# Performance work log

Hardware: AMD Instinct MI355X
Metric: run time of the kernel (lower is better)

## Reference

```python
import jax, jax.numpy as jnp
import numpy as np

B_SZ, T, H, N, L = 4, 512, 256, 64, 4
EPS = 1e-5

def _hippo(n):
    i = np.arange(n)[:, None]; j = np.arange(n)[None, :]
    A = np.where(i >= j, ((-1.0) ** (i - j)) * np.sqrt((2 * i + 1.0) * (2 * j + 1.0)), 0.0)
    # scale to be contractive so the 512-step dense recurrence stays finite
    A = A / (1.1 * np.linalg.norm(A, 2))
    return A.astype(np.float32)

def _xavier(key, shape):
    fan_in, fan_out = shape[1], shape[0]
    a = float(np.sqrt(6.0 / (fan_in + fan_out)))
    return jax.random.uniform(key, shape, jnp.float32, -a, a)

def setup_inputs() -> dict:
    key = jax.random.key(0)
    ks = jax.random.split(key, 8)
    x = jax.random.normal(ks[0], (B_SZ, T, H), jnp.float32)
    A = jnp.broadcast_to(jnp.asarray(_hippo(N)), (L, N, N))
    Bm = jnp.stack([_xavier(jax.random.fold_in(ks[1], l), (N, H)) for l in range(L)])
    Cm = jnp.stack([_xavier(jax.random.fold_in(ks[2], l), (H, N)) for l in range(L)])
    Dm = jnp.stack([_xavier(jax.random.fold_in(ks[3], l), (H, H)) for l in range(L)])
    Win = _xavier(ks[4], (H, H)); bin_ = jnp.zeros((H,), jnp.float32)
    Wout = _xavier(ks[5], (H, H)); bout = jnp.zeros((H,), jnp.float32)
    return {"x": x, "Win": Win, "bin_": bin_, "Wout": Wout, "bout": bout,
            "A": A, "Bm": Bm, "Cm": Cm, "Dm": Dm}

def _ln(x):
    m = jnp.mean(x, -1, keepdims=True)
    v = jnp.mean((x - m) ** 2, -1, keepdims=True)
    return (x - m) / jnp.sqrt(v + EPS)

def _ssm_layer(h, A, B, C, D):
    # h: (B,T,H); dense state (B,N,H)
    Cbar = C.mean(0)            # mean over output rows (matches C_state.mean(dim=2))
    BT = B.T                    # (H,N)
    DT = D.T                    # (H,H)
    def step(state, u):        # state (B,N,H), u (B,H)
        y = jnp.einsum('bnh,n->bh', state, Cbar) + u @ DT   # output uses pre-update state
        new_state = jnp.einsum('nm,bmh->bnh', A, state) + (u @ BT)[:, :, None]
        return new_state, y
    state0 = jnp.zeros((h.shape[0], A.shape[0], h.shape[2]), h.dtype)
    _, ys = jax.lax.scan(step, state0, jnp.swapaxes(h, 0, 1))  # scan over T
    y = jnp.swapaxes(ys, 0, 1)
    y = jax.nn.gelu(y, approximate=False) + h   # GELU -> (dropout=0) -> residual
    return _ln(y)

def reference(x, Win, bin_, Wout, bout, A, Bm, Cm, Dm):
    h = x @ Win.T + bin_
    for l in range(L):
        h = _ssm_layer(h, A[l], Bm[l], Cm[l], Dm[l])
    h = _ln(h)
    return h @ Wout.T + bout
```

## Files before the change

kernel.cpp:

```cpp
#include <hip/hip_runtime.h>

#define TSEQ 512
#define HDIM 256
#define NDIM 64
#define LC   48
#define YSTR 260

typedef __attribute__((ext_vector_type(4))) float  f32x4;
typedef __attribute__((ext_vector_type(8))) short  s16x8;
typedef __attribute__((ext_vector_type(4))) unsigned short u16x4;
typedef unsigned long long u64;
typedef unsigned short us;

#define MFMA16 __builtin_amdgcn_mfma_f32_16x16x32_bf16

__device__ __forceinline__ float wave_red(float v) {
#pragma unroll
    for (int m = 1; m < 64; m <<= 1) v += __shfl_xor(v, m, 64);
    return v;
}
__device__ __forceinline__ float lane_bcast(float v, int l) {
    return __int_as_float(__builtin_amdgcn_readlane(__float_as_int(v), l));
}
__device__ __forceinline__ us f2bf(float f) {
    unsigned u = __float_as_uint(f);
    u += 0x7fffu + ((u >> 16) & 1u);
    return (us)(u >> 16);
}
__device__ __forceinline__ float bf2f(us h) {
    return __uint_as_float(((unsigned)h) << 16);
}
__device__ __forceinline__ int swz(int row, int chunk) {
    return row * 512 + (((chunk) ^ (row & 7)) << 4);
}

__global__ void __launch_bounds__(256) k_prep(
    const float* __restrict__ Win, const float* __restrict__ Wout,
    const float* __restrict__ Bm, const float* __restrict__ Dm,
    const float* __restrict__ Cm, const float* __restrict__ A,
    us* __restrict__ Win_bf, us* __restrict__ Wout_bf,
    us* __restrict__ Bm_bf, us* __restrict__ Dm_bf,
    float* __restrict__ cbar_g, float* __restrict__ wA8)
{
    __shared__ __align__(16) float Pa[4096];
    __shared__ __align__(16) float Pb[4096];
    const int gid = blockIdx.x, tid = threadIdx.x;

    if (gid < 128) {
        for (int q = gid * 256 + tid; q < 114688; q += 32768) {
            const float* s; us* d; int off;
            if (q < 16384)      { s = Win;  d = Win_bf;  off = q; }
            else if (q < 32768) { s = Wout; d = Wout_bf; off = q - 16384; }
            else if (q < 49152) { s = Bm;   d = Bm_bf;   off = q - 32768; }
            else                { s = Dm;   d = Dm_bf;   off = q - 49152; }
            f32x4 v = ((const f32x4*)s)[off];
            u16x4 p; p[0] = f2bf(v[0]); p[1] = f2bf(v[1]); p[2] = f2bf(v[2]); p[3] = f2bf(v[3]);
            ((u16x4*)d)[off] = p;
        }
        return;
    }
    if (gid == 128) {
        const int l = tid >> 6, n = tid & 63;
        const float* cp = Cm + (size_t)l * HDIM * NDIM + n;
        float s0 = 0.f, s1 = 0.f, s2 = 0.f, s3 = 0.f;
        for (int h = 0; h < HDIM; h += 4) {
            s0 += cp[(h + 0) * NDIM]; s1 += cp[(h + 1) * NDIM];
            s2 += cp[(h + 2) * NDIM]; s3 += cp[(h + 3) * NDIM];
        }
        cbar_g[tid] = ((s0 + s1) + (s2 + s3)) * (1.0f / HDIM);
        return;
    }
    for (int q = tid; q < 1024; q += 256) ((f32x4*)Pa)[q] = ((const f32x4*)A)[q];
    __syncthreads();
    const int r0 = (tid >> 3) * 2, c0 = (tid & 7) * 8;
    const f32x4 z4 = {0.f, 0.f, 0.f, 0.f};
#pragma unroll 1
    for (int it = 0; it < 3; ++it) {
        const float* S = (it & 1) ? Pb : Pa;
        float*       D = (it & 1) ? Pa : Pb;
        f32x4 s00 = z4, s01 = z4, s10 = z4, s11 = z4;
        for (int k = 0; k < 64; ++k) {
            float a0 = S[r0 * 64 + k], a1 = S[(r0 + 1) * 64 + k];
            f32x4 b0 = *(const f32x4*)(S + k * 64 + c0);
            f32x4 b1 = *(const f32x4*)(S + k * 64 + c0 + 4);
            s00 += a0 * b0; s01 += a0 * b1; s10 += a1 * b0; s11 += a1 * b1;
        }
        *(f32x4*)(D + r0 * 64 + c0) = s00;       *(f32x4*)(D + r0 * 64 + c0 + 4) = s01;
        *(f32x4*)(D + (r0 + 1) * 64 + c0) = s10; *(f32x4*)(D + (r0 + 1) * 64 + c0 + 4) = s11;
        __syncthreads();
    }
    for (int q = tid; q < 1024; q += 256) ((f32x4*)wA8)[q] = ((const f32x4*)Pb)[q];
}

__global__ void __launch_bounds__(512, 2) k_front(
    const float* __restrict__ x, const float* __restrict__ bin,
    const us* __restrict__ Win_bf, const us* __restrict__ Bm_bf,
    const float* __restrict__ A, const float* __restrict__ wA8,
    const float* __restrict__ cbar_g,
    us* __restrict__ hA, float* __restrict__ binpA, float* __restrict__ wbuf)
{
    __shared__ __align__(16) float sm[13312];
    us* xl = (us*)sm;

    const int gid = blockIdx.x, tid = threadIdx.x;
    const int lane = tid & 63, wv = tid >> 6;
    const int m = lane & 15, cgq = lane >> 4;
    const f32x4 z4 = {0.f, 0.f, 0.f, 0.f};

    if (gid == 128) {
        float* As  = sm;
        float* A8s = sm + 4096;
        float* uls = sm + 8192;
        for (int q = tid; q < 1024; q += 512) {
            ((f32x4*)As)[q]  = ((const f32x4*)A)[q];
            ((f32x4*)A8s)[q] = ((const f32x4*)wA8)[q];
        }
        __syncthreads();
        if (wv < 4) {
            const int l = wv;
            float u = cbar_g[l * 64 + lane];
            uls[(l * 8 + 0) * 64 + lane] = u;
#pragma unroll 1
            for (int s = 1; s < 8; ++s) {
                float p0 = 0.f, p1 = 0.f, p2 = 0.f, p3 = 0.f;
#pragma unroll
                for (int k = 0; k < 64; k += 4) {
                    p0 += As[(k + 0) * 64 + lane] * lane_bcast(u, k + 0);
                    p1 += As[(k + 1) * 64 + lane] * lane_bcast(u, k + 1);
                    p2 += As[(k + 2) * 64 + lane] * lane_bcast(u, k + 2);
                    p3 += As[(k + 3) * 64 + lane] * lane_bcast(u, k + 3);
                }
                u = (p0 + p1) + (p2 + p3);
                uls[(l * 8 + s) * 64 + lane] = u;
            }
        }
        __syncthreads();
        {
            const int p = wv;
            float u0 = uls[(0 * 8 + p) * 64 + lane];
            float u1 = uls[(1 * 8 + p) * 64 + lane];
            float u2 = uls[(2 * 8 + p) * 64 + lane];
            float u3 = uls[(3 * 8 + p) * 64 + lane];
#pragma unroll 1
            for (int k6 = 0; k6 < 6; ++k6) {
                const int j = p + 8 * k6;
                wbuf[(0 * LC + j) * 64 + lane] = u0;
                wbuf[(1 * LC + j) * 64 + lane] = u1;
                wbuf[(2 * LC + j) * 64 + lane] = u2;
                wbuf[(3 * LC + j) * 64 + lane] = u3;
                if (k6 < 5) {
                    float n0 = 0.f, n1 = 0.f, n2 = 0.f, n3 = 0.f;
#pragma unroll
                    for (int k = 0; k < 64; ++k) {
                        float a = A8s[k * 64 + lane];
                        n0 += a * lane_bcast(u0, k); n1 += a * lane_bcast(u1, k);
                        n2 += a * lane_bcast(u2, k); n3 += a * lane_bcast(u3, k);
                    }
                    u0 = n0; u1 = n1; u2 = n2; u3 = n3;
                }
            }
        }
        return;
    }

    const int b = gid >> 5, tb = gid & 31, t0 = tb * 16;
    const size_t grow = (size_t)(b * TSEQ + t0);

    {
        const f32x4* gs = (const f32x4*)(x + grow * HDIM);
#pragma unroll
        for (int k = 0; k < 2; ++k) {
            int q = tid + k * 512;
            int row = q >> 6, c4 = q & 63;
            f32x4 v = gs[q];
            u16x4 pk; pk[0] = f2bf(v[0]); pk[1] = f2bf(v[1]); pk[2] = f2bf(v[2]); pk[3] = f2bf(v[3]);
            *(u16x4*)((char*)xl + swz(row, c4 >> 1) + (c4 & 1) * 8) = pk;
        }
    }
    __syncthreads();

    {
        f32x4 accA = z4, accB = z4;
        const us* W0 = Win_bf + (size_t)(wv * 32 + m) * HDIM;
        const us* W1 = Win_bf + (size_t)(wv * 32 + 16 + m) * HDIM;
#pragma unroll
        for (int ks = 0; ks < 8; ++ks) {
            s16x8 av = *(const s16x8*)((const char*)xl + swz(m, ks * 4 + cgq));
            s16x8 b0 = *(const s16x8*)(W0 + ks * 32 + cgq * 8);
            s16x8 b1 = *(const s16x8*)(W1 + ks * 32 + cgq * 8);
            accA = MFMA16(av, b0, accA, 0, 0, 0);
            accB = MFMA16(av, b1, accB, 0, 0, 0);
        }
        __syncthreads();
        const int h0c = wv * 32 + m, h1c = wv * 32 + 16 + m;
        float bi0 = bin[h0c], bi1 = bin[h1c];
#pragma unroll
        for (int reg = 0; reg < 4; ++reg) {
            int trow = cgq * 4 + reg;
            *(us*)((char*)xl + swz(trow, h0c >> 3) + (h0c & 7) * 2) = f2bf(accA[reg] + bi0);
            *(us*)((char*)xl + swz(trow, h1c >> 3) + (h1c & 7) * 2) = f2bf(accB[reg] + bi1);
        }
    }
    __syncthreads();

    {
        us* gd = hA + grow * HDIM;
#pragma unroll
        for (int k = 0; k < 2; ++k) {
            int q = tid + k * 512;
            int row = q >> 6, c8 = q & 63;
            *(u16x4*)(gd + (size_t)row * HDIM + c8 * 4) =
                *(const u16x4*)((const char*)xl + swz(row, c8 >> 1) + (c8 & 1) * 8);
        }
    }
    if (wv < 4) {
        f32x4 accb = z4;
        const us* B0 = Bm_bf + (size_t)(wv * 16 + m) * HDIM;
#pragma unroll
        for (int ks = 0; ks < 8; ++ks) {
            s16x8 av = *(const s16x8*)((const char*)xl + swz(m, ks * 4 + cgq));
            s16x8 bv = *(const s16x8*)(B0 + ks * 32 + cgq * 8);
            accb = MFMA16(av, bv, accb, 0, 0, 0);
        }
#pragma unroll
        for (int reg = 0; reg < 4; ++reg)
            binpA[(grow + cgq * 4 + reg) * NDIM + wv * 16 + m] = accb[reg];
    }
}

template <bool LAST>
__global__ void __launch_bounds__(512, 2) k_layer(
    const us* __restrict__ hin, const float* __restrict__ binp_in,
    const float* __restrict__ wbuf_l, const us* __restrict__ Dl_bf,
    const us* __restrict__ Bn_bf, const us* __restrict__ Wout_bf,
    const float* __restrict__ bout,
    us* __restrict__ hout, float* __restrict__ binp_out, float* __restrict__ out)
{
    __shared__ __align__(16) us    xl[16 * HDIM];
    __shared__ __align__(16) float yl[16 * YSTR];
    __shared__ __align__(16) float bwin[64 * NDIM];
    __shared__ __align__(16) float wlds[LC * NDIM];
    __shared__ float cfin[16];

    const int gid = blockIdx.x, tid = threadIdx.x;
    const int lane = tid & 63, wv = tid >> 6;
    const int m = lane & 15, cgq = lane >> 4;
    const f32x4 z4 = {0.f, 0.f, 0.f, 0.f};
    const int b = gid >> 5, tb = gid & 31, t0 = tb * 16;
    const size_t grow = (size_t)(b * TSEQ + t0);

    {
        const us* gs = hin + grow * HDIM;
#pragma unroll
        for (int k = 0; k < 2; ++k) {
            int q = tid + k * 512;
            int row = q >> 6, c8 = q & 63;
            *(u16x4*)((char*)xl + swz(row, c8 >> 1) + (c8 & 1) * 8) =
                *(const u16x4*)(gs + (size_t)row * HDIM + c8 * 4);
        }
    }
    for (int q = tid; q < LC * NDIM / 4; q += 512)
        ((f32x4*)wlds)[q] = ((const f32x4*)wbuf_l)[q];
    {
        const u64* bi8 = (const u64*)(binp_in + (size_t)b * TSEQ * NDIM);
#pragma unroll
        for (int k = 0; k < 4; ++k) {
            int q = tid + k * 512;
            int r = q >> 5, cc = q & 31;
            int t = t0 - LC + r;
            ((u64*)bwin)[q] = (t >= 0) ? bi8[(size_t)t * 32 + cc] : 0ull;
        }
    }
    __syncthreads();

    f32x4 accA = z4, accB = z4;
    {
        const us* D0 = Dl_bf + (size_t)(wv * 32 + m) * HDIM;
        const us* D1 = Dl_bf + (size_t)(wv * 32 + 16 + m) * HDIM;
#pragma unroll
        for (int ks = 0; ks < 8; ++ks) {
            s16x8 av = *(const s16x8*)((const char*)xl + swz(m, ks * 4 + cgq));
            s16x8 b0 = *(const s16x8*)(D0 + ks * 32 + cgq * 8);
            s16x8 b1 = *(const s16x8*)(D1 + ks * 32 + cgq * 8);
            accA = MFMA16(av, b0, accA, 0, 0, 0);
            accB = MFMA16(av, b1, accB, 0, 0, 0);
        }
    }

    {
        const int r0 = wv * 2;
        float c0 = 0.f, c1 = 0.f;
        float v0 = bwin[(LC - 1 + r0) * NDIM + lane];
        float v1 = bwin[(LC + r0) * NDIM + lane];
#pragma unroll
        for (int j = 0; j < LC; ++j) {
            float wj = wlds[j * NDIM + lane];
            c0 += wj * v0; c1 += wj * v1;
            v1 = v0;
            int nr = LC - 2 + r0 - j; nr = nr < 0 ? 0 : nr;
            v0 = bwin[nr * NDIM + lane];
        }
        c0 = wave_red(c0); c1 = wave_red(c1);
        if (lane == 0) { cfin[r0] = c0; cfin[r0 + 1] = c1; }
    }
    __syncthreads();

#pragma unroll
    for (int nt = 0; nt < 2; ++nt) {
        int hcol = wv * 32 + nt * 16 + m;
#pragma unroll
        for (int reg = 0; reg < 4; ++reg) {
            int trow = cgq * 4 + reg;
            float val = (nt ? accB[reg] : accA[reg]) + cfin[trow];
            float g = 0.5f * val * (1.0f + erff(val * 0.70710678118654752f));
            float r = bf2f(*(const us*)((const char*)xl + swz(trow, hcol >> 3) + (hcol & 7) * 2));
            yl[trow * YSTR + hcol] = g + r;
        }
    }
    __syncthreads();

#pragma unroll
    for (int q = 0; q < 2; ++q) {
        int r = wv * 2 + q;
        f32x4 yv = *(const f32x4*)(yl + r * YSTR + lane * 4);
        float s = (yv[0] + yv[1]) + (yv[2] + yv[3]);
        float sq = yv[0] * yv[0] + yv[1] * yv[1] + yv[2] * yv[2] + yv[3] * yv[3];
        s = wave_red(s); sq = wave_red(sq);
        float mn = s * (1.0f / HDIM);
        float var = sq * (1.0f / HDIM) - mn * mn;
        float rs = rsqrtf(var + 1e-5f);
        if (LAST) { float vz = var * rs * rs; rs = rs * rsqrtf(vz + 1e-5f); }
        u16x4 zp;
        zp[0] = f2bf((yv[0] - mn) * rs); zp[1] = f2bf((yv[1] - mn) * rs);
        zp[2] = f2bf((yv[2] - mn) * rs); zp[3] = f2bf((yv[3] - mn) * rs);
        *(u16x4*)((char*)xl + swz(r, lane >> 1) + (lane & 1) * 8) = zp;
        if constexpr (!LAST)
            *(u16x4*)(hout + (grow + r) * HDIM + lane * 4) = zp;
    }
    __syncthreads();

    if constexpr (!LAST) {
        if (wv < 4) {
            f32x4 accb = z4;
            const us* B0 = Bn_bf + (size_t)(wv * 16 + m) * HDIM;
#pragma unroll
            for (int ks = 0; ks < 8; ++ks) {
                s16x8 av = *(const s16x8*)((const char*)xl + swz(m, ks * 4 + cgq));
                s16x8 bv = *(const s16x8*)(B0 + ks * 32 + cgq * 8);
                accb = MFMA16(av, bv, accb, 0, 0, 0);
            }
#pragma unroll
            for (int reg = 0; reg < 4; ++reg)
                binp_out[(grow + cgq * 4 + reg) * NDIM + wv * 16 + m] = accb[reg];
        }
    } else {
        f32x4 a2A = z4, a2B = z4;
        const us* W0 = Wout_bf + (size_t)(wv * 32 + m) * HDIM;
        const us* W1 = Wout_bf + (size_t)(wv * 32 + 16 + m) * HDIM;
#pragma unroll
        for (int ks = 0; ks < 8; ++ks) {
            s16x8 av = *(const s16x8*)((const char*)xl + swz(m, ks * 4 + cgq));
            s16x8 b0 = *(const s16x8*)(W0 + ks * 32 + cgq * 8);
            s16x8 b1 = *(const s16x8*)(W1 + ks * 32 + cgq * 8);
            a2A = MFMA16(av, b0, a2A, 0, 0, 0);
            a2B = MFMA16(av, b1, a2B, 0, 0, 0);
        }
#pragma unroll
        for (int nt = 0; nt < 2; ++nt) {
            int hcol = wv * 32 + nt * 16 + m;
            float bo = bout[hcol];
#pragma unroll
            for (int reg = 0; reg < 4; ++reg) {
                int trow = cgq * 4 + reg;
                out[(grow + trow) * HDIM + hcol] = (nt ? a2B[reg] : a2A[reg]) + bo;
            }
        }
    }
}

extern "C" void kernel_launch(void* const* d_in, const int* in_sizes, int n_in,
                              void* d_out, int out_size, void* d_ws, size_t ws_size,
                              hipStream_t stream) {
    (void)in_sizes; (void)n_in; (void)out_size; (void)ws_size;
    const float* x    = (const float*)d_in[0];
    const float* Win  = (const float*)d_in[1];
    const float* bin  = (const float*)d_in[2];
    const float* Wout = (const float*)d_in[3];
    const float* bout = (const float*)d_in[4];
    const float* A    = (const float*)d_in[5];
    const float* Bm   = (const float*)d_in[6];
    const float* Cm   = (const float*)d_in[7];
    const float* Dm   = (const float*)d_in[8];

    float* ws     = (float*)d_ws;
    float* wbuf   = ws;
    float* cbar_g = ws + 16384;
    float* wA8    = ws + 17408;
    float* biA    = ws + 21504;
    float* biB    = ws + 152576;
    us* Win_bf  = (us*)(ws + 283648);
    us* Wout_bf = Win_bf + 65536;
    us* Bm_bf   = Wout_bf + 65536;
    us* Dm_bf   = Bm_bf + 65536;
    us* hA      = Dm_bf + 262144;
    us* hB      = hA + 524288;
    float* out  = (float*)d_out;

    k_prep<<<130, 256, 0, stream>>>(Win, Wout, Bm, Dm, Cm, A,
                                    Win_bf, Wout_bf, Bm_bf, Dm_bf, cbar_g, wA8);
    k_front<<<129, 512, 0, stream>>>(x, bin, Win_bf, Bm_bf, A, wA8, cbar_g,
                                     hA, biA, wbuf);
    k_layer<false><<<128, 512, 0, stream>>>(hA, biA, wbuf + 0 * LC * NDIM,
        Dm_bf + (size_t)0 * 65536, Bm_bf + (size_t)1 * 16384, nullptr, nullptr,
        hB, biB, nullptr);
    k_layer<false><<<128, 512, 0, stream>>>(hB, biB, wbuf + 1 * LC * NDIM,
        Dm_bf + (size_t)1 * 65536, Bm_bf + (size_t)2 * 16384, nullptr, nullptr,
        hA, biA, nullptr);
    k_layer<false><<<128, 512, 0, stream>>>(hA, biA, wbuf + 2 * LC * NDIM,
        Dm_bf + (size_t)2 * 65536, Bm_bf + (size_t)3 * 16384, nullptr, nullptr,
        hB, biB, nullptr);
    k_layer<true><<<128, 512, 0, stream>>>(hB, biB, wbuf + 3 * LC * NDIM,
        Dm_bf + (size_t)3 * 65536, nullptr, Wout_bf, bout,
        nullptr, nullptr, out);
}
```

Measured before the change: 73.98 us.

## Fuse front and four layer kernels into one persistent kernel with flag sync

Merges the front projection and the four per-layer launches into a single kernel of 129 blocks. Each block keeps its 16-row activation tile in LDS across layers and waits only on agent-scope flags from the three preceding time blocks and from the kernel-weight block, instead of a full grid barrier at each launch boundary. This drops the bf16 h round-trips through global memory and four launch gaps. In exchange it relies on all 129 blocks being co-resident so the spin-waits cannot deadlock, and on relaxed atomics for cross-block visibility, which costs extra polling latency.

After: 71.94 us. 1.03x faster.

```diff
diff --git a/kernel.cpp b/kernel.cpp
--- a/kernel.cpp
+++ b/kernel.cpp
@@ -5,6 +5,7 @@
 #define NDIM 64
 #define LC   48
 #define YSTR 260
+#define NWB  128
 
 typedef __attribute__((ext_vector_type(4))) float  f32x4;
 typedef __attribute__((ext_vector_type(8))) short  s16x8;
@@ -32,6 +33,20 @@
 }
 __device__ __forceinline__ int swz(int row, int chunk) {
     return row * 512 + (((chunk) ^ (row & 7)) << 4);
+}
+
+__device__ __forceinline__ void st_mall(float* p, float v) {
+    __hip_atomic_store(p, v, __ATOMIC_RELAXED, __HIP_MEMORY_SCOPE_AGENT);
+}
+__device__ __forceinline__ u64 ld_mall8(const u64* p) {
+    return __hip_atomic_load(p, __ATOMIC_RELAXED, __HIP_MEMORY_SCOPE_AGENT);
+}
+__device__ __forceinline__ void flag_set(unsigned* f) {
+    __hip_atomic_store(f, 1u, __ATOMIC_RELAXED, __HIP_MEMORY_SCOPE_AGENT);
+}
+__device__ __forceinline__ void flag_wait(const unsigned* f) {
+    while (__hip_atomic_load(f, __ATOMIC_RELAXED, __HIP_MEMORY_SCOPE_AGENT) == 0u)
+        __builtin_amdgcn_s_sleep(1);
 }
 
 __global__ void __launch_bounds__(256) k_prep(
@@ -40,7 +55,8 @@
     const float* __restrict__ Cm, const float* __restrict__ A,
     us* __restrict__ Win_bf, us* __restrict__ Wout_bf,
     us* __restrict__ Bm_bf, us* __restrict__ Dm_bf,
-    float* __restrict__ cbar_g, float* __restrict__ wA8)
+    float* __restrict__ cbar_g, float* __restrict__ wA8,
+    unsigned* __restrict__ flags)
 {
     __shared__ __align__(16) float Pa[4096];
     __shared__ __align__(16) float Pb[4096];
@@ -60,6 +76,8 @@
         return;
     }
     if (gid == 128) {
+        for (int i = tid; i < 4 + 4 * NWB; i += 256)
+            __hip_atomic_store(&flags[i], 0u, __ATOMIC_RELAXED, __HIP_MEMORY_SCOPE_AGENT);
         const int l = tid >> 6, n = tid & 63;
         const float* cp = Cm + (size_t)l * HDIM * NDIM + n;
         float s0 = 0.f, s1 = 0.f, s2 = 0.f, s3 = 0.f;
@@ -92,25 +110,31 @@
     for (int q = tid; q < 1024; q += 256) ((f32x4*)wA8)[q] = ((const f32x4*)Pb)[q];
 }
 
-__global__ void __launch_bounds__(512, 2) k_front(
+__global__ void __launch_bounds__(512, 2) k_fused(
     const float* __restrict__ x, const float* __restrict__ bin,
-    const us* __restrict__ Win_bf, const us* __restrict__ Bm_bf,
-    const float* __restrict__ A, const float* __restrict__ wA8,
-    const float* __restrict__ cbar_g,
-    us* __restrict__ hA, float* __restrict__ binpA, float* __restrict__ wbuf)
+    const float* __restrict__ bout, const float* __restrict__ A,
+    const float* __restrict__ wA8, const float* __restrict__ cbar_g,
+    const us* __restrict__ Win_bf, const us* __restrict__ Wout_bf,
+    const us* __restrict__ Bm_bf, const us* __restrict__ Dm_bf,
+    float* __restrict__ wbuf, float* __restrict__ BiA, float* __restrict__ BiB,
+    unsigned* __restrict__ flags, float* __restrict__ out)
 {
-    __shared__ __align__(16) float sm[13312];
-    us* xl = (us*)sm;
+    __shared__ __align__(16) char smem[53568];
+    us*    xl   = (us*)smem;
+    float* yl   = (float*)(smem + 8192);
+    float* bwin = (float*)(smem + 24832);
+    float* wlds = (float*)(smem + 41216);
+    float* cfin = (float*)(smem + 53504);
 
     const int gid = blockIdx.x, tid = threadIdx.x;
     const int lane = tid & 63, wv = tid >> 6;
     const int m = lane & 15, cgq = lane >> 4;
     const f32x4 z4 = {0.f, 0.f, 0.f, 0.f};
 
-    if (gid == 128) {
-        float* As  = sm;
-        float* A8s = sm + 4096;
-        float* uls = sm + 8192;
+    if (gid == NWB) {
+        float* As  = (float*)smem;
+        float* A8s = (float*)(smem + 16384);
+        float* uls = (float*)(smem + 32768);
         for (int q = tid; q < 1024; q += 512) {
             ((f32x4*)As)[q]  = ((const f32x4*)A)[q];
             ((f32x4*)A8s)[q] = ((const f32x4*)wA8)[q];
@@ -144,10 +168,10 @@
 #pragma unroll 1
             for (int k6 = 0; k6 < 6; ++k6) {
                 const int j = p + 8 * k6;
-                wbuf[(0 * LC + j) * 64 + lane] = u0;
-                wbuf[(1 * LC + j) * 64 + lane] = u1;
-                wbuf[(2 * LC + j) * 64 + lane] = u2;
-                wbuf[(3 * LC + j) * 64 + lane] = u3;
+                st_mall(&wbuf[(0 * LC + j) * 64 + lane], u0);
+                st_mall(&wbuf[(1 * LC + j) * 64 + lane], u1);
+                st_mall(&wbuf[(2 * LC + j) * 64 + lane], u2);
+                st_mall(&wbuf[(3 * LC + j) * 64 + lane], u3);
                 if (k6 < 5) {
                     float n0 = 0.f, n1 = 0.f, n2 = 0.f, n3 = 0.f;
 #pragma unroll
@@ -160,6 +184,8 @@
                 }
             }
         }
+        __syncthreads();
+        if (tid < 4) flag_set(&flags[tid]);
         return;
     }
 
@@ -203,16 +229,6 @@
     }
     __syncthreads();
 
-    {
-        us* gd = hA + grow * HDIM;
-#pragma unroll
-        for (int k = 0; k < 2; ++k) {
-            int q = tid + k * 512;
-            int row = q >> 6, c8 = q & 63;
-            *(u16x4*)(gd + (size_t)row * HDIM + c8 * 4) =
-                *(const u16x4*)((const char*)xl + swz(row, c8 >> 1) + (c8 & 1) * 8);
-        }
-    }
     if (wv < 4) {
         f32x4 accb = z4;
         const us* B0 = Bm_bf + (size_t)(wv * 16 + m) * HDIM;
@@ -224,155 +240,143 @@
         }
 #pragma unroll
         for (int reg = 0; reg < 4; ++reg)
-            binpA[(grow + cgq * 4 + reg) * NDIM + wv * 16 + m] = accb[reg];
-    }
-}
-
-template <bool LAST>
-__global__ void __launch_bounds__(512, 2) k_layer(
-    const us* __restrict__ hin, const float* __restrict__ binp_in,
-    const float* __restrict__ wbuf_l, const us* __restrict__ Dl_bf,
-    const us* __restrict__ Bn_bf, const us* __restrict__ Wout_bf,
-    const float* __restrict__ bout,
-    us* __restrict__ hout, float* __restrict__ binp_out, float* __restrict__ out)
-{
-    __shared__ __align__(16) us    xl[16 * HDIM];
-    __shared__ __align__(16) float yl[16 * YSTR];
-    __shared__ __align__(16) float bwin[64 * NDIM];
-    __shared__ __align__(16) float wlds[LC * NDIM];
-    __shared__ float cfin[16];
-
-    const int gid = blockIdx.x, tid = threadIdx.x;
-    const int lane = tid & 63, wv = tid >> 6;
-    const int m = lane & 15, cgq = lane >> 4;
-    const f32x4 z4 = {0.f, 0.f, 0.f, 0.f};
-    const int b = gid >> 5, tb = gid & 31, t0 = tb * 16;
-    const size_t grow = (size_t)(b * TSEQ + t0);
-
-    {
-        const us* gs = hin + grow * HDIM;
-#pragma unroll
-        for (int k = 0; k < 2; ++k) {
-            int q = tid + k * 512;
-            int row = q >> 6, c8 = q & 63;
-            *(u16x4*)((char*)xl + swz(row, c8 >> 1) + (c8 & 1) * 8) =
-                *(const u16x4*)(gs + (size_t)row * HDIM + c8 * 4);
-        }
-    }
-    for (int q = tid; q < LC * NDIM / 4; q += 512)
-        ((f32x4*)wlds)[q] = ((const f32x4*)wbuf_l)[q];
-    {
-        const u64* bi8 = (const u64*)(binp_in + (size_t)b * TSEQ * NDIM);
-#pragma unroll
-        for (int k = 0; k < 4; ++k) {
-            int q = tid + k * 512;
-            int r = q >> 5, cc = q & 31;
-            int t = t0 - LC + r;
-            ((u64*)bwin)[q] = (t >= 0) ? bi8[(size_t)t * 32 + cc] : 0ull;
-        }
+            st_mall(&BiA[(grow + cgq * 4 + reg) * NDIM + wv * 16 + m], accb[reg]);
     }
     __syncthreads();
-
-    f32x4 accA = z4, accB = z4;
-    {
-        const us* D0 = Dl_bf + (size_t)(wv * 32 + m) * HDIM;
-        const us* D1 = Dl_bf + (size_t)(wv * 32 + 16 + m) * HDIM;
-#pragma unroll
-        for (int ks = 0; ks < 8; ++ks) {
-            s16x8 av = *(const s16x8*)((const char*)xl + swz(m, ks * 4 + cgq));
-            s16x8 b0 = *(const s16x8*)(D0 + ks * 32 + cgq * 8);
-            s16x8 b1 = *(const s16x8*)(D1 + ks * 32 + cgq * 8);
-            accA = MFMA16(av, b0, accA, 0, 0, 0);
-            accB = MFMA16(av, b1, accB, 0, 0, 0);
-        }
-    }
-
-    {
-        const int r0 = wv * 2;
-        float c0 = 0.f, c1 = 0.f;
-        float v0 = bwin[(LC - 1 + r0) * NDIM + lane];
-        float v1 = bwin[(LC + r0) * NDIM + lane];
-#pragma unroll
-        for (int j = 0; j < LC; ++j) {
-            float wj = wlds[j * NDIM + lane];
-            c0 += wj * v0; c1 += wj * v1;
-            v1 = v0;
-            int nr = LC - 2 + r0 - j; nr = nr < 0 ? 0 : nr;
-            v0 = bwin[nr * NDIM + lane];
-        }
-        c0 = wave_red(c0); c1 = wave_red(c1);
-        if (lane == 0) { cfin[r0] = c0; cfin[r0 + 1] = c1; }
-    }
-    __syncthreads();
-
-#pragma unroll
-    for (int nt = 0; nt < 2; ++nt) {
-        int hcol = wv * 32 + nt * 16 + m;
-#pragma unroll
-        for (int reg = 0; reg < 4; ++reg) {
-            int trow = cgq * 4 + reg;
-            float val = (nt ? accB[reg] : accA[reg]) + cfin[trow];
-            float g = 0.5f * val * (1.0f + erff(val * 0.70710678118654752f));
-            float r = bf2f(*(const us*)((const char*)xl + swz(trow, hcol >> 3) + (hcol & 7) * 2));
-            yl[trow * YSTR + hcol] = g + r;
-        }
-    }
-    __syncthreads();
-
-#pragma unroll
-    for (int q = 0; q < 2; ++q) {
-        int r = wv * 2 + q;
-        f32x4 yv = *(const f32x4*)(yl + r * YSTR + lane * 4);
-        float s = (yv[0] + yv[1]) + (yv[2] + yv[3]);
-        float sq = yv[0] * yv[0] + yv[1] * yv[1] + yv[2] * yv[2] + yv[3] * yv[3];
-        s = wave_red(s); sq = wave_red(sq);
-        float mn = s * (1.0f / HDIM);
-        float var = sq * (1.0f / HDIM) - mn * mn;
-        float rs = rsqrtf(var + 1e-5f);
-        if (LAST) { float vz = var * rs * rs; rs = rs * rsqrtf(vz + 1e-5f); }
-        u16x4 zp;
-        zp[0] = f2bf((yv[0] - mn) * rs); zp[1] = f2bf((yv[1] - mn) * rs);
-        zp[2] = f2bf((yv[2] - mn) * rs); zp[3] = f2bf((yv[3] - mn) * rs);
-        *(u16x4*)((char*)xl + swz(r, lane >> 1) + (lane & 1) * 8) = zp;
-        if constexpr (!LAST)
-            *(u16x4*)(hout + (grow + r) * HDIM + lane * 4) = zp;
-    }
-    __syncthreads();
-
-    if constexpr (!LAST) {
-        if (wv < 4) {
-            f32x4 accb = z4;
-            const us* B0 = Bn_bf + (size_t)(wv * 16 + m) * HDIM;
+    if (tid == 0) flag_set(&flags[4 + 0 * NWB + gid]);
+
+#pragma unroll 1
+    for (int l = 0; l < 4; ++l) {
+        const us* Dl = Dm_bf + (size_t)l * HDIM * HDIM;
+        const float* bi = (l & 1) ? BiB : BiA;
+        float*       bo = (l & 1) ? BiA : BiB;
+
+        f32x4 accA = z4, accB = z4;
+        {
+            const us* D0 = Dl + (size_t)(wv * 32 + m) * HDIM;
+            const us* D1 = Dl + (size_t)(wv * 32 + 16 + m) * HDIM;
 #pragma unroll
             for (int ks = 0; ks < 8; ++ks) {
                 s16x8 av = *(const s16x8*)((const char*)xl + swz(m, ks * 4 + cgq));
-                s16x8 bv = *(const s16x8*)(B0 + ks * 32 + cgq * 8);
-                accb = MFMA16(av, bv, accb, 0, 0, 0);
-            }
-#pragma unroll
-            for (int reg = 0; reg < 4; ++reg)
-                binp_out[(grow + cgq * 4 + reg) * NDIM + wv * 16 + m] = accb[reg];
-        }
-    } else {
-        f32x4 a2A = z4, a2B = z4;
-        const us* W0 = Wout_bf + (size_t)(wv * 32 + m) * HDIM;
-        const us* W1 = Wout_bf + (size_t)(wv * 32 + 16 + m) * HDIM;
-#pragma unroll
-        for (int ks = 0; ks < 8; ++ks) {
-            s16x8 av = *(const s16x8*)((const char*)xl + swz(m, ks * 4 + cgq));
-            s16x8 b0 = *(const s16x8*)(W0 + ks * 32 + cgq * 8);
-            s16x8 b1 = *(const s16x8*)(W1 + ks * 32 + cgq * 8);
-            a2A = MFMA16(av, b0, a2A, 0, 0, 0);
-            a2B = MFMA16(av, b1, a2B, 0, 0, 0);
-        }
+                s16x8 b0 = *(const s16x8*)(D0 + ks * 32 + cgq * 8);
+                s16x8 b1 = *(const s16x8*)(D1 + ks * 32 + cgq * 8);
+                accA = MFMA16(av, b0, accA, 0, 0, 0);
+                accB = MFMA16(av, b1, accB, 0, 0, 0);
+            }
+        }
+
+        {
+            const unsigned* fp = nullptr;
+            if (lane == 3) fp = &flags[l];
+            else if (lane < 3 && (tb - 1 - (int)lane) >= 0) fp = &flags[4 + l * NWB + gid - 1 - lane];
+            if (fp) flag_wait(fp);
+        }
+
+        {
+            const u64* ws8 = (const u64*)(wbuf + (size_t)l * LC * NDIM);
+            for (int q = tid; q < LC * NDIM / 2; q += 512)
+                ((u64*)wlds)[q] = ld_mall8(&ws8[q]);
+            const u64* bi8 = (const u64*)(bi + (size_t)b * TSEQ * NDIM);
+#pragma unroll
+            for (int k = 0; k < 4; ++k) {
+                int q = tid + k * 512;
+                int r = q >> 5, cc = q & 31;
+                int t = t0 - LC + r;
+                ((u64*)bwin)[q] = (t >= 0) ? ld_mall8(&bi8[(size_t)t * 32 + cc]) : 0ull;
+            }
+        }
+        __syncthreads();
+
+        {
+            const int r0 = wv * 2;
+            float c0 = 0.f, c1 = 0.f;
+            float v0 = bwin[(LC - 1 + r0) * NDIM + lane];
+            float v1 = bwin[(LC + r0) * NDIM + lane];
+#pragma unroll
+            for (int j = 0; j < LC; ++j) {
+                float wj = wlds[j * NDIM + lane];
+                c0 += wj * v0; c1 += wj * v1;
+                v1 = v0;
+                int nr = LC - 2 + r0 - j; nr = nr < 0 ? 0 : nr;
+                v0 = bwin[nr * NDIM + lane];
+            }
+            c0 = wave_red(c0); c1 = wave_red(c1);
+            if (lane == 0) { cfin[r0] = c0; cfin[r0 + 1] = c1; }
+        }
+        __syncthreads();
+
 #pragma unroll
         for (int nt = 0; nt < 2; ++nt) {
             int hcol = wv * 32 + nt * 16 + m;
-            float bo = bout[hcol];
 #pragma unroll
             for (int reg = 0; reg < 4; ++reg) {
                 int trow = cgq * 4 + reg;
-                out[(grow + trow) * HDIM + hcol] = (nt ? a2B[reg] : a2A[reg]) + bo;
+                float val = (nt ? accB[reg] : accA[reg]) + cfin[trow];
+                float g = 0.5f * val * (1.0f + erff(val * 0.70710678118654752f));
+                float r = bf2f(*(const us*)((const char*)xl + swz(trow, hcol >> 3) + (hcol & 7) * 2));
+                yl[trow * YSTR + hcol] = g + r;
+            }
+        }
+        __syncthreads();
+
+        {
+            const bool last = (l == 3);
+#pragma unroll
+            for (int q = 0; q < 2; ++q) {
+                int r = wv * 2 + q;
+                f32x4 yv = *(const f32x4*)(yl + r * YSTR + lane * 4);
+                float s = (yv[0] + yv[1]) + (yv[2] + yv[3]);
+                float sq = yv[0] * yv[0] + yv[1] * yv[1] + yv[2] * yv[2] + yv[3] * yv[3];
+                s = wave_red(s); sq = wave_red(sq);
+                float mn = s * (1.0f / HDIM);
+                float var = sq * (1.0f / HDIM) - mn * mn;
+                float rs = rsqrtf(var + 1e-5f);
+                if (last) { float vz = var * rs * rs; rs = rs * rsqrtf(vz + 1e-5f); }
+                u16x4 zp;
+                zp[0] = f2bf((yv[0] - mn) * rs); zp[1] = f2bf((yv[1] - mn) * rs);
+                zp[2] = f2bf((yv[2] - mn) * rs); zp[3] = f2bf((yv[3] - mn) * rs);
+                *(u16x4*)((char*)xl + swz(r, lane >> 1) + (lane & 1) * 8) = zp;
+            }
+        }
+        __syncthreads();
+
+        if (l < 3) {
+            if (wv < 4) {
+                f32x4 accb = z4;
+                const us* B0 = Bm_bf + (size_t)(l + 1) * NDIM * HDIM + (size_t)(wv * 16 + m) * HDIM;
+#pragma unroll
+                for (int ks = 0; ks < 8; ++ks) {
+                    s16x8 av = *(const s16x8*)((const char*)xl + swz(m, ks * 4 + cgq));
+                    s16x8 bv = *(const s16x8*)(B0 + ks * 32 + cgq * 8);
+                    accb = MFMA16(av, bv, accb, 0, 0, 0);
+                }
+#pragma unroll
+                for (int reg = 0; reg < 4; ++reg)
+                    st_mall(&bo[(grow + cgq * 4 + reg) * NDIM + wv * 16 + m], accb[reg]);
+            }
+            __syncthreads();
+            if (tid == 0) flag_set(&flags[4 + (l + 1) * NWB + gid]);
+        } else {
+            f32x4 a2A = z4, a2B = z4;
+            const us* W0 = Wout_bf + (size_t)(wv * 32 + m) * HDIM;
+            const us* W1 = Wout_bf + (size_t)(wv * 32 + 16 + m) * HDIM;
+#pragma unroll
+            for (int ks = 0; ks < 8; ++ks) {
+                s16x8 av = *(const s16x8*)((const char*)xl + swz(m, ks * 4 + cgq));
+                s16x8 b0 = *(const s16x8*)(W0 + ks * 32 + cgq * 8);
+                s16x8 b1 = *(const s16x8*)(W1 + ks * 32 + cgq * 8);
+                a2A = MFMA16(av, b0, a2A, 0, 0, 0);
+                a2B = MFMA16(av, b1, a2B, 0, 0, 0);
+            }
+#pragma unroll
+            for (int nt = 0; nt < 2; ++nt) {
+                int hcol = wv * 32 + nt * 16 + m;
+                float bo2 = bout[hcol];
+#pragma unroll
+                for (int reg = 0; reg < 4; ++reg) {
+                    int trow = cgq * 4 + reg;
+                    out[(grow + trow) * HDIM + hcol] = (nt ? a2B[reg] : a2A[reg]) + bo2;
+                }
             }
         }
     }
@@ -398,28 +402,16 @@
     float* wA8    = ws + 17408;
     float* biA    = ws + 21504;
     float* biB    = ws + 152576;
-    us* Win_bf  = (us*)(ws + 283648);
+    unsigned* flags = (unsigned*)(ws + 283648);
+    us* Win_bf  = (us*)(ws + 284672);
     us* Wout_bf = Win_bf + 65536;
     us* Bm_bf   = Wout_bf + 65536;
     us* Dm_bf   = Bm_bf + 65536;
-    us* hA      = Dm_bf + 262144;
-    us* hB      = hA + 524288;
     float* out  = (float*)d_out;
 
     k_prep<<<130, 256, 0, stream>>>(Win, Wout, Bm, Dm, Cm, A,
-                                    Win_bf, Wout_bf, Bm_bf, Dm_bf, cbar_g, wA8);
-    k_front<<<129, 512, 0, stream>>>(x, bin, Win_bf, Bm_bf, A, wA8, cbar_g,
-                                     hA, biA, wbuf);
-    k_layer<false><<<128, 512, 0, stream>>>(hA, biA, wbuf + 0 * LC * NDIM,
-        Dm_bf + (size_t)0 * 65536, Bm_bf + (size_t)1 * 16384, nullptr, nullptr,
-        hB, biB, nullptr);
-    k_layer<false><<<128, 512, 0, stream>>>(hB, biB, wbuf + 1 * LC * NDIM,
-        Dm_bf + (size_t)1 * 65536, Bm_bf + (size_t)2 * 16384, nullptr, nullptr,
-        hA, biA, nullptr);
-    k_layer<false><<<128, 512, 0, stream>>>(hA, biA, wbuf + 2 * LC * NDIM,
-        Dm_bf + (size_t)2 * 65536, Bm_bf + (size_t)3 * 16384, nullptr, nullptr,
-        hB, biB, nullptr);
-    k_layer<true><<<128, 512, 0, stream>>>(hB, biB, wbuf + 3 * LC * NDIM,
-        Dm_bf + (size_t)3 * 65536, nullptr, Wout_bf, bout,
-        nullptr, nullptr, out);
-}
+                                    Win_bf, Wout_bf, Bm_bf, Dm_bf, cbar_g, wA8, flags);
+    k_fused<<<NWB + 1, 512, 0, stream>>>(x, bin, bout, A, wA8, cbar_g,
+                                         Win_bf, Wout_bf, Bm_bf, Dm_bf,
+                                         wbuf, biA, biB, flags, out);
+}
```
